# Kernel optimization log

Hardware: AMD Instinct MI355X
Metric: run time of the kernel (lower is better)

The kernel has to match this reference:

```python
import jax, jax.numpy as jnp
import numpy as np

B, S, HID = 2, 2048, 2048
NH, NKV, HD = 16, 4, 128
GROUPS = NH // NKV
CLIP = 8.0
ROPE_THETA = 500000.0
QKV_OUT = HID + 2 * NKV * HD  # 3072
NEG = jnp.finfo(jnp.float32).min


def setup_inputs() -> dict:
    key = jax.random.key(0)
    k1, k2, k3 = jax.random.split(key, 3)
    hidden_states = jax.random.normal(k1, (B, S, HID), dtype=jnp.float32)
    position_ids = jnp.tile(jnp.arange(S, dtype=jnp.int64)[None, :], (B, 1))
    Wqkv = jax.random.normal(k2, (QKV_OUT, HID), dtype=jnp.float32) * (HID ** -0.5)
    Wout = jax.random.normal(k3, (HID, HID), dtype=jnp.float32) * (HID ** -0.5)
    return {"hidden_states": hidden_states, "position_ids": position_ids,
            "Wqkv": Wqkv, "Wout": Wout}


def _rotate_half(x):
    x1, x2 = jnp.split(x, 2, axis=-1)
    return jnp.concatenate((-x2, x1), axis=-1)


def reference(hidden_states, position_ids, Wqkv, Wout):
    b, s, _ = hidden_states.shape
    # fused QKV projection + clamp
    qkv = jnp.einsum('bsh,oh->bso', hidden_states, Wqkv)
    qkv = jnp.clip(qkv, -CLIP, CLIP)
    q, k, v = jnp.split(qkv, [HID, HID + NKV * HD], axis=2)
    q = q.reshape(b, s, NH, HD).transpose(0, 2, 1, 3)   # [b, nh, s, hd]
    k = k.reshape(b, s, NKV, HD).transpose(0, 2, 1, 3)  # [b, nkv, s, hd]
    v = v.reshape(b, s, NKV, HD).transpose(0, 2, 1, 3)
    # rotary embedding
    inv_freq = 1.0 / (ROPE_THETA ** (jnp.arange(0, HD, 2, dtype=jnp.float32) / HD))
    freqs = position_ids.astype(jnp.float32)[:, :, None] * inv_freq[None, None, :]  # [b,s,hd/2]
    emb = jnp.concatenate((freqs, freqs), axis=-1)      # [b, s, hd]
    cos = jnp.cos(emb)[:, None, :, :]                   # [b, 1, s, hd]
    sin = jnp.sin(emb)[:, None, :, :]
    q = q * cos + _rotate_half(q) * sin
    k = k * cos + _rotate_half(k) * sin
    # repeat kv heads (GQA)
    k = jnp.repeat(k, GROUPS, axis=1)  # [b, nh, s, hd]
    v = jnp.repeat(v, GROUPS, axis=1)
    # attention with additive causal mask
    scores = jnp.einsum('bhqd,bhkd->bhqk', q, k) / jnp.sqrt(jnp.float32(HD))
    causal = jnp.where(jnp.tril(jnp.ones((s, s), dtype=bool)), 0.0, NEG)
    scores = scores + causal[None, None, :, :]
    attn = jax.nn.softmax(scores.astype(jnp.float32), axis=-1).astype(q.dtype)
    out = jnp.einsum('bhqk,bhkd->bhqd', attn, v)
    out = out.transpose(0, 2, 1, 3).reshape(b, s, HID)
    return jnp.einsum('bsh,oh->bso', out, Wout)
```

## Files before the change

### kernel.cpp

```cpp
#include <hip/hip_runtime.h>
#include <stdint.h>

#define S_    2048
#define HID_  2048
#define NH_   16
#define NKV_  4
#define HD_   128

using short4x = __attribute__((ext_vector_type(4))) short;
using short8  = __attribute__((ext_vector_type(8))) short;
using floatx4 = __attribute__((ext_vector_type(4))) float;

#define NEGBIG (-3.0e38f)
#define QSCL_  (0.08838834764831845f * 1.4426950408889634f)

__device__ __forceinline__ unsigned short f2bf(float x) {
  union { float f; unsigned u; } v; v.f = x;
  unsigned r = v.u + 0x7fffu + ((v.u >> 16) & 1u);
  return (unsigned short)(r >> 16);
}
__device__ __forceinline__ void ld_lds16(const void* g, void* l) {
  __builtin_amdgcn_global_load_lds(
      (const __attribute__((address_space(1))) unsigned*)g,
      (__attribute__((address_space(3))) unsigned*)l, 16, 0, 0);
}

__global__ void k_cvt3(const float* __restrict__ s0, unsigned short* __restrict__ d0, int n0,
                       const float* __restrict__ s1, unsigned short* __restrict__ d1, int n1,
                       const float* __restrict__ s2, unsigned short* __restrict__ d2, int n2) {
  int i = blockIdx.x * blockDim.x + threadIdx.x;
  const float* s; unsigned short* d;
  if (i < n0) { s = s0; d = d0; }
  else if (i < n0 + n1) { s = s1; d = d1; i -= n0; }
  else { s = s2; d = d2; i -= n0 + n1; if (i >= n2) return; }
  float4 v = ((const float4*)s)[i];
  union { unsigned short us[4]; uint2 u2; } u;
  u.us[0] = f2bf(v.x); u.us[1] = f2bf(v.y); u.us[2] = f2bf(v.z); u.us[3] = f2bf(v.w);
  ((uint2*)d)[i] = u.u2;
}

template <int EPI>
__global__ void __launch_bounds__(256)
k_gemm_bt(const unsigned short* __restrict__ A, const unsigned short* __restrict__ Bw,
          unsigned short* __restrict__ Qb, unsigned short* __restrict__ Kb,
          unsigned short* __restrict__ Vt, float* __restrict__ Of,
          const int* __restrict__ pos) {
  const int K = HID_;
  __shared__ __align__(16) unsigned short As[128 * 32];
  __shared__ __align__(16) unsigned short Bs[128 * 32];
  const int tid  = threadIdx.x;
  const int wave = tid >> 6, lane = tid & 63;
  const int quad = lane >> 4, l15 = lane & 15;
  const int wm = (wave >> 1) * 64;
  const int bc2 = (wave & 1) * 32;
  const int m0 = blockIdx.x * 128, n0 = blockIdx.y * 128;

  floatx4 acc[4][4] = {};

  const int srow = tid >> 2;
  const int scol = (tid & 3) * 8;
  const unsigned short* Ag0 = A  + (size_t)(m0 + srow)      * K + scol;
  const unsigned short* Ag1 = A  + (size_t)(m0 + 64 + srow) * K + scol;
  const unsigned short* Bg0 = Bw + (size_t)(n0 + srow)      * K + scol;
  const unsigned short* Bg1 = Bw + (size_t)(n0 + 64 + srow) * K + scol;
  unsigned short* lA0 = &As[tid * 8];
  unsigned short* lA1 = &As[2048 + tid * 8];
  unsigned short* lB0 = &Bs[tid * 8];
  unsigned short* lB1 = &Bs[2048 + tid * 8];

  for (int k0 = 0; k0 < K; k0 += 32) {
    __syncthreads();
    ld_lds16(Ag0 + k0, lA0);
    ld_lds16(Ag1 + k0, lA1);
    ld_lds16(Bg0 + k0, lB0);
    ld_lds16(Bg1 + k0, lB1);
    __syncthreads();
    short8 a[4], b[4];
#pragma unroll
    for (int i = 0; i < 4; i++) a[i] = *(const short8*)&As[(wm + i * 16 + l15) * 32 + quad * 8];
#pragma unroll
    for (int j = 0; j < 4; j++) {
      const int brow = bc2 + (j & 1) * 16 + (j >> 1) * 64;
      b[j] = *(const short8*)&Bs[(brow + l15) * 32 + quad * 8];
    }
#pragma unroll
    for (int i = 0; i < 4; i++)
#pragma unroll
      for (int j = 0; j < 4; j++)
        acc[i][j] = __builtin_amdgcn_mfma_f32_16x16x32_bf16(a[i], b[j], acc[i][j], 0, 0, 0);
  }

  if (EPI == 1) {
#pragma unroll
    for (int i = 0; i < 4; i++)
#pragma unroll
      for (int j = 0; j < 4; j++) {
        const int col = n0 + bc2 + (j & 1) * 16 + (j >> 1) * 64 + l15;
#pragma unroll
        for (int r = 0; r < 4; r++) {
          const int row = m0 + wm + i * 16 + quad * 4 + r;
          Of[(size_t)row * HID_ + col] = acc[i][j][r];
        }
      }
    return;
  }

  if (n0 >= HID_ + NKV_ * HD_) {
#pragma unroll
    for (int i = 0; i < 4; i++)
#pragma unroll
      for (int j = 0; j < 4; j++) {
        const int col = n0 + bc2 + (j & 1) * 16 + (j >> 1) * 64 + l15;
        const int oo = col - (HID_ + NKV_ * HD_);
        const int kvh = oo >> 7, d = oo & 127;
#pragma unroll
        for (int r = 0; r < 4; r++) {
          const int row = m0 + wm + i * 16 + quad * 4 + r;
          float x = fminf(fmaxf(acc[i][j][r], -8.0f), 8.0f);
          int bb = row >> 11, ss = row & 2047;
          Vt[((size_t)((bb * NKV_ + kvh) * HD_ + d) << 11) + ss] = f2bf(x);
        }
      }
    return;
  }

  const bool isQ = (n0 < HID_);
  const float oscale = isQ ? QSCL_ : 1.0f;
  float inv2p[2];
#pragma unroll
  for (int j = 0; j < 2; j++) {
    const float d = (float)(bc2 + j * 16 + l15);
    inv2p[j] = __builtin_amdgcn_exp2f(-d * 0.29580575865f) * 0.15915494309189535f;
  }
#pragma unroll
  for (int i = 0; i < 4; i++) {
    const int rowb = m0 + wm + i * 16 + quad * 4;
#pragma unroll
    for (int r = 0; r < 4; r++) {
      const int row = rowb + r;
      const float p = (float)pos[row];
#pragma unroll
      for (int j = 0; j < 2; j++) {
        const int dlo = bc2 + j * 16 + l15;
        const float rv = __builtin_amdgcn_fractf(p * inv2p[j]);
        const float cs = __builtin_amdgcn_cosf(rv);
        const float sn = __builtin_amdgcn_sinf(rv);
        const float x = fminf(fmaxf(acc[i][j][r],     -8.0f), 8.0f);
        const float y = fminf(fmaxf(acc[i][j + 2][r], -8.0f), 8.0f);
        const float lo = (x * cs - y * sn) * oscale;
        const float hi = (y * cs + x * sn) * oscale;
        if (isQ) {
          Qb[(size_t)row * HID_ + n0 + dlo]      = f2bf(lo);
          Qb[(size_t)row * HID_ + n0 + dlo + 64] = f2bf(hi);
        } else {
          const int cb = n0 - HID_;
          Kb[(size_t)row * (NKV_ * HD_) + cb + dlo]      = f2bf(lo);
          Kb[(size_t)row * (NKV_ * HD_) + cb + dlo + 64] = f2bf(hi);
        }
      }
    }
  }
}

__global__ void __launch_bounds__(256, 2)
k_attn(const unsigned short* __restrict__ Qb, const unsigned short* __restrict__ Kb,
       const unsigned short* __restrict__ Vt, unsigned short* __restrict__ AO) {
  __shared__ __align__(16) unsigned short sm[2][16384];
  __shared__ __align__(16) unsigned short Pl[4][16][88];

  const int tid  = threadIdx.x;
  const int wave = tid >> 6, lane = tid & 63;
  const int quad = lane >> 4, l15 = lane & 15;
  const int tLow  = blockIdx.x;
  const int tHigh = 31 - tLow;
  const int q0L = tLow * 64, q0H = tHigh * 64;
  const int bh = blockIdx.y;
  const int b = bh >> 4, h = bh & 15;
  const int kvh = h >> 2;

  const int srow = tid >> 2;
  const int scolz = (((tid & 3) ^ ((tid >> 3) & 3)) * 8);
  const int qoff = ((quad ^ ((l15 >> 1) & 3)) * 8);

  {
    const unsigned short* qgL = Qb + (size_t)(b * S_ + q0L + srow) * HID_ + h * HD_ + scolz;
    const unsigned short* qgH = Qb + (size_t)(b * S_ + q0H + srow) * HID_ + h * HD_ + scolz;
#pragma unroll
    for (int i = 0; i < 4; i++) ld_lds16(qgL + i * 32, &sm[0][i * 2048 + tid * 8]);
#pragma unroll
    for (int i = 0; i < 4; i++) ld_lds16(qgH + i * 32, &sm[1][i * 2048 + tid * 8]);
  }
  __syncthreads();
  short8 qaL[4], qaH[4];
#pragma unroll
  for (int c = 0; c < 4; c++) {
    qaL[c] = *(const short8*)&sm[0][(c * 64 + wave * 16 + l15) * 32 + qoff];
    qaH[c] = *(const short8*)&sm[1][(c * 64 + wave * 16 + l15) * 32 + qoff];
  }
  __syncthreads();

  floatx4 oacL[8] = {}, oacH[8] = {};
  floatx4 oacEL = {}, oacEH = {};
  float mL = NEGBIG, mH = NEGBIG;

  const unsigned short* kgb = Kb + (size_t)b * S_ * (NKV_ * HD_) + kvh * HD_ + scolz;
  const unsigned short* vgb = Vt + (size_t)(b * NKV_ + kvh) * HD_ * S_;

  unsigned short* PlW = &Pl[wave][0][0];

  short8 ones;
#pragma unroll
  for (int i = 0; i < 8; i++) ones[i] = (short)0x3F80;

  auto stage = [&](int bufI, int j) {
    unsigned short* B = &sm[bufI][0];
    const unsigned short* kg = kgb + (size_t)(j * 64 + srow) * (NKV_ * HD_);
#pragma unroll
    for (int i = 0; i < 4; i++) ld_lds16(kg + i * 32, &B[i * 2048 + tid * 8]);
#pragma unroll
    for (int i = 0; i < 4; i++) {
      int c = i >> 1, rowd = (i & 1) * 64 + srow;
      ld_lds16(vgb + (size_t)rowd * S_ + j * 64 + c * 32 + scolz,
               &B[8192 + c * 4096 + (i & 1) * 2048 + tid * 8]);
    }
  };

  auto softmax_tile = [&](floatx4* sc, floatx4* oac, floatx4& oacE, float& m_run,
                          int q0, int j, bool diag, short8& pa0, short8& pa1) {
    if (diag) {
      const int rowq = q0 + wave * 16 + l15;
#pragma unroll
      for (int t = 0; t < 4; t++) {
        const int kb0 = j * 64 + t * 16 + quad * 4;
#pragma unroll
        for (int r = 0; r < 4; r++)
          if (kb0 + r > rowq) sc[t][r] = NEGBIG;
      }
    }
    float mx = sc[0][0];
#pragma unroll
    for (int t = 0; t < 4; t++)
#pragma unroll
      for (int r = 0; r < 4; r++) mx = fmaxf(mx, sc[t][r]);
    mx = fmaxf(mx, __shfl_xor(mx, 16));
    mx = fmaxf(mx, __shfl_xor(mx, 32));

    const float mo = m_run;
    if (__any(mx > mo + 8.0f)) {
      m_run = fmaxf(mo, mx);
      float alpha = __builtin_amdgcn_exp2f(mo - m_run);
      float al4[4];
#pragma unroll
      for (int r = 0; r < 4; r++) al4[r] = __shfl(alpha, quad * 4 + r, 16);
#pragma unroll
      for (int t = 0; t < 8; t++)
#pragma unroll
        for (int r = 0; r < 4; r++) oac[t][r] *= al4[r];
#pragma unroll
      for (int r = 0; r < 4; r++) oacE[r] *= al4[r];
    }
#pragma unroll
    for (int t = 0; t < 4; t++) {
      short4x pk;
#pragma unroll
      for (int r = 0; r < 4; r++)
        pk[r] = (short)f2bf(__builtin_amdgcn_exp2f(sc[t][r] - m_run));
      *(short4x*)&PlW[l15 * 88 + t * 16 + quad * 4] = pk;
    }
    pa0 = *(const short8*)&PlW[l15 * 88 + quad * 8];
    pa1 = *(const short8*)&PlW[l15 * 88 + 32 + quad * 8];
  };

  auto step_two = [&](int j, const unsigned short* Kt, const unsigned short* Vts,
                      bool diagL, bool diagH) {
    floatx4 scH[4] = {}, scL[4] = {};
    __builtin_amdgcn_s_setprio(1);
#pragma unroll
    for (int t = 0; t < 4; t++)
#pragma unroll
      for (int c = 0; c < 4; c++) {
        short8 ka = *(const short8*)&Kt[c * 2048 + (t * 16 + l15) * 32 + qoff];
        scH[t] = __builtin_amdgcn_mfma_f32_16x16x32_bf16(ka, qaH[c], scH[t], 0, 0, 0);
        scL[t] = __builtin_amdgcn_mfma_f32_16x16x32_bf16(ka, qaL[c], scL[t], 0, 0, 0);
      }
    __builtin_amdgcn_s_setprio(0);
    short8 paH0, paH1, paL0, paL1;
    softmax_tile(scH, oacH, oacEH, mH, q0H, j, diagH, paH0, paH1);
    softmax_tile(scL, oacL, oacEL, mL, q0L, j, diagL, paL0, paL1);
    __builtin_amdgcn_s_setprio(1);
#pragma unroll
    for (int t = 0; t < 8; t++) {
      short8 vb0 = *(const short8*)&Vts[(t * 16 + l15) * 32 + qoff];
      oacH[t] = __builtin_amdgcn_mfma_f32_16x16x32_bf16(paH0, vb0, oacH[t], 0, 0, 0);
      oacL[t] = __builtin_amdgcn_mfma_f32_16x16x32_bf16(paL0, vb0, oacL[t], 0, 0, 0);
      short8 vb1 = *(const short8*)&Vts[4096 + (t * 16 + l15) * 32 + qoff];
      oacH[t] = __builtin_amdgcn_mfma_f32_16x16x32_bf16(paH1, vb1, oacH[t], 0, 0, 0);
      oacL[t] = __builtin_amdgcn_mfma_f32_16x16x32_bf16(paL1, vb1, oacL[t], 0, 0, 0);
    }
    oacEH = __builtin_amdgcn_mfma_f32_16x16x32_bf16(paH0, ones, oacEH, 0, 0, 0);
    oacEH = __builtin_amdgcn_mfma_f32_16x16x32_bf16(paH1, ones, oacEH, 0, 0, 0);
    oacEL = __builtin_amdgcn_mfma_f32_16x16x32_bf16(paL0, ones, oacEL, 0, 0, 0);
    oacEL = __builtin_amdgcn_mfma_f32_16x16x32_bf16(paL1, ones, oacEL, 0, 0, 0);
    __builtin_amdgcn_s_setprio(0);
  };

  auto step_one = [&](int j, const unsigned short* Kt, const unsigned short* Vts, bool diagH) {
    floatx4 scH[4] = {};
    __builtin_amdgcn_s_setprio(1);
#pragma unroll
    for (int t = 0; t < 4; t++)
#pragma unroll
      for (int c = 0; c < 4; c++) {
        short8 ka = *(const short8*)&Kt[c * 2048 + (t * 16 + l15) * 32 + qoff];
        scH[t] = __builtin_amdgcn_mfma_f32_16x16x32_bf16(ka, qaH[c], scH[t], 0, 0, 0);
      }
    __builtin_amdgcn_s_setprio(0);
    short8 paH0, paH1;
    softmax_tile(scH, oacH, oacEH, mH, q0H, j, diagH, paH0, paH1);
    __builtin_amdgcn_s_setprio(1);
#pragma unroll
    for (int t = 0; t < 8; t++) {
      short8 vb0 = *(const short8*)&Vts[(t * 16 + l15) * 32 + qoff];
      oacH[t] = __builtin_amdgcn_mfma_f32_16x16x32_bf16(paH0, vb0, oacH[t], 0, 0, 0);
      short8 vb1 = *(const short8*)&Vts[4096 + (t * 16 + l15) * 32 + qoff];
      oacH[t] = __builtin_amdgcn_mfma_f32_16x16x32_bf16(paH1, vb1, oacH[t], 0, 0, 0);
    }
    oacEH = __builtin_amdgcn_mfma_f32_16x16x32_bf16(paH0, ones, oacEH, 0, 0, 0);
    oacEH = __builtin_amdgcn_mfma_f32_16x16x32_bf16(paH1, ones, oacEH, 0, 0, 0);
    __builtin_amdgcn_s_setprio(0);
  };

  stage(0, 0);
  int cur = 0;
  for (int j = 0; j <= tHigh; ++j) {
    __syncthreads();
    if (j < tHigh) stage(cur ^ 1, j + 1);
    const unsigned short* Kt  = &sm[cur][0];
    const unsigned short* Vts = Kt + 8192;
    if (j <= tLow) step_two(j, Kt, Vts, j == tLow, j == tHigh);
    else           step_one(j, Kt, Vts, j == tHigh);
    cur ^= 1;
  }

#pragma unroll
  for (int t = 0; t < 8; t++)
#pragma unroll
    for (int r = 0; r < 4; r++) {
      int rgL = q0L + wave * 16 + quad * 4 + r;
      int rgH = q0H + wave * 16 + quad * 4 + r;
      AO[(size_t)(b * S_ + rgL) * HID_ + h * HD_ + t * 16 + l15] = f2bf(oacL[t][r] / oacEL[r]);
      AO[(size_t)(b * S_ + rgH) * HID_ + h * HD_ + t * 16 + l15] = f2bf(oacH[t][r] / oacEH[r]);
    }
}

extern "C" void kernel_launch(void* const* d_in, const int* in_sizes, int n_in,
                              void* d_out, int out_size, void* d_ws, size_t ws_size,
                              hipStream_t stream) {
  (void)in_sizes; (void)n_in; (void)out_size; (void)ws_size;
  const float* hidden = (const float*)d_in[0];
  const int*   pos    = (const int*)d_in[1];
  const float* Wqkv   = (const float*)d_in[2];
  const float* Wout   = (const float*)d_in[3];
  float* out = (float*)d_out;

  unsigned short* ws = (unsigned short*)d_ws;
  const size_t M1 = 1024 * 1024;
  unsigned short* hb  = ws;
  unsigned short* wqb = ws + 8 * M1;
  unsigned short* wob = ws + 14 * M1;
  unsigned short* Qb  = ws + 18 * M1;
  unsigned short* Kb  = ws + 26 * M1;
  unsigned short* Vt  = ws + 28 * M1;
  unsigned short* AO  = hb;

  k_cvt3<<<18432, 256, 0, stream>>>(hidden, hb, 2097152,
                                    Wqkv, wqb, 1572864,
                                    Wout, wob, 1048576);
  k_gemm_bt<0><<<dim3(32, 24), 256, 0, stream>>>(hb, wqb, Qb, Kb, Vt, nullptr, pos);
  k_attn<<<dim3(16, 32), 256, 0, stream>>>(Qb, Kb, Vt, AO);
  k_gemm_bt<1><<<dim3(32, 16), 256, 0, stream>>>(AO, wob, nullptr, nullptr, nullptr, out, nullptr);
}
```

Baseline: 290.0 us.

## Single-buffer K/V in LDS and raise attention occupancy to four blocks per CU

Replaces the double-buffered K/V shared-memory tiles with one buffer, which roughly halves LDS use, and raises launch bounds from 2 to 4 blocks per CU. The load of the next tile no longer overlaps compute: each iteration now stages the tile and waits on an extra barrier before the MFMAs, relying on more resident waves to hide latency. The P scratch tile also shrinks from a padded 88-element row stride to 64 with an XOR swizzle meant to avoid bank conflicts. The tighter register budget under the new launch bounds risks spills given the large accumulator arrays.

```diff
diff --git a/kernel.cpp b/kernel.cpp
--- a/kernel.cpp
+++ b/kernel.cpp
@@ -162,11 +162,11 @@
   }
 }
 
-__global__ void __launch_bounds__(256, 2)
+__global__ void __launch_bounds__(256, 4)
 k_attn(const unsigned short* __restrict__ Qb, const unsigned short* __restrict__ Kb,
        const unsigned short* __restrict__ Vt, unsigned short* __restrict__ AO) {
-  __shared__ __align__(16) unsigned short sm[2][16384];
-  __shared__ __align__(16) unsigned short Pl[4][16][88];
+  __shared__ __align__(16) unsigned short sm[16384];
+  __shared__ __align__(16) unsigned short Pl[4][16][64];
 
   const int tid  = threadIdx.x;
   const int wave = tid >> 6, lane = tid & 63;
@@ -186,16 +186,16 @@
     const unsigned short* qgL = Qb + (size_t)(b * S_ + q0L + srow) * HID_ + h * HD_ + scolz;
     const unsigned short* qgH = Qb + (size_t)(b * S_ + q0H + srow) * HID_ + h * HD_ + scolz;
 #pragma unroll
-    for (int i = 0; i < 4; i++) ld_lds16(qgL + i * 32, &sm[0][i * 2048 + tid * 8]);
-#pragma unroll
-    for (int i = 0; i < 4; i++) ld_lds16(qgH + i * 32, &sm[1][i * 2048 + tid * 8]);
+    for (int i = 0; i < 4; i++) ld_lds16(qgL + i * 32, &sm[i * 2048 + tid * 8]);
+#pragma unroll
+    for (int i = 0; i < 4; i++) ld_lds16(qgH + i * 32, &sm[8192 + i * 2048 + tid * 8]);
   }
   __syncthreads();
   short8 qaL[4], qaH[4];
 #pragma unroll
   for (int c = 0; c < 4; c++) {
-    qaL[c] = *(const short8*)&sm[0][(c * 64 + wave * 16 + l15) * 32 + qoff];
-    qaH[c] = *(const short8*)&sm[1][(c * 64 + wave * 16 + l15) * 32 + qoff];
+    qaL[c] = *(const short8*)&sm[(c * 64 + wave * 16 + l15) * 32 + qoff];
+    qaH[c] = *(const short8*)&sm[8192 + (c * 64 + wave * 16 + l15) * 32 + qoff];
   }
   __syncthreads();
 
@@ -212,16 +212,15 @@
 #pragma unroll
   for (int i = 0; i < 8; i++) ones[i] = (short)0x3F80;
 
-  auto stage = [&](int bufI, int j) {
-    unsigned short* B = &sm[bufI][0];
+  auto stage = [&](int j) {
     const unsigned short* kg = kgb + (size_t)(j * 64 + srow) * (NKV_ * HD_);
 #pragma unroll
-    for (int i = 0; i < 4; i++) ld_lds16(kg + i * 32, &B[i * 2048 + tid * 8]);
+    for (int i = 0; i < 4; i++) ld_lds16(kg + i * 32, &sm[i * 2048 + tid * 8]);
 #pragma unroll
     for (int i = 0; i < 4; i++) {
       int c = i >> 1, rowd = (i & 1) * 64 + srow;
       ld_lds16(vgb + (size_t)rowd * S_ + j * 64 + c * 32 + scolz,
-               &B[8192 + c * 4096 + (i & 1) * 2048 + tid * 8]);
+               &sm[8192 + c * 4096 + (i & 1) * 2048 + tid * 8]);
     }
   };
 
@@ -259,16 +258,17 @@
 #pragma unroll
       for (int r = 0; r < 4; r++) oacE[r] *= al4[r];
     }
+    const int swz = l15 & 7;
 #pragma unroll
     for (int t = 0; t < 4; t++) {
       short4x pk;
 #pragma unroll
       for (int r = 0; r < 4; r++)
         pk[r] = (short)f2bf(__builtin_amdgcn_exp2f(sc[t][r] - m_run));
-      *(short4x*)&PlW[l15 * 88 + t * 16 + quad * 4] = pk;
-    }
-    pa0 = *(const short8*)&PlW[l15 * 88 + quad * 8];
-    pa1 = *(const short8*)&PlW[l15 * 88 + 32 + quad * 8];
+      *(short4x*)&PlW[l15 * 64 + (((t * 2 + (quad >> 1)) ^ swz) * 8) + (quad & 1) * 4] = pk;
+    }
+    pa0 = *(const short8*)&PlW[l15 * 64 + ((quad ^ swz) * 8)];
+    pa1 = *(const short8*)&PlW[l15 * 64 + (((4 + quad) ^ swz) * 8)];
   };
 
   auto step_two = [&](int j, const unsigned short* Kt, const unsigned short* Vts,
@@ -330,16 +330,14 @@
     __builtin_amdgcn_s_setprio(0);
   };
 
-  stage(0, 0);
-  int cur = 0;
+  const unsigned short* Kt  = sm;
+  const unsigned short* Vts = sm + 8192;
   for (int j = 0; j <= tHigh; ++j) {
     __syncthreads();
-    if (j < tHigh) stage(cur ^ 1, j + 1);
-    const unsigned short* Kt  = &sm[cur][0];
-    const unsigned short* Vts = Kt + 8192;
+    stage(j);
+    __syncthreads();
     if (j <= tLow) step_two(j, Kt, Vts, j == tLow, j == tHigh);
     else           step_one(j, Kt, Vts, j == tHigh);
-    cur ^= 1;
   }
 
 #pragma unroll
```

After: 582.9 us. 101% more time.
